# Kernel optimization log

Measured on AMD Instinct MI355X. Metric: run time of the kernel, lower is better.

The kernel has to match this reference:

```python
import jax, jax.numpy as jnp
import numpy as np

B, L, C, H, T = 4096, 32, 28, 512, 32


def setup_inputs() -> dict:
    key = jax.random.key(0)
    ks = jax.random.split(key, 10)
    s = 0.1
    return dict(
        input=jax.random.normal(ks[0], (B, L, C), jnp.float32),
        unpacked_masks=jnp.ones((B, L, 1), jnp.float32),
        bias_mat=jax.random.normal(ks[1], (B, L), jnp.float32),
        conv1_w=jax.random.normal(ks[2], (C, C, 3), jnp.float32) * s,  # OIH
        conv1_b=jnp.zeros((C,), jnp.float32),
        conv_w=jax.random.normal(ks[3], (1, C, 1), jnp.float32) * s,
        conv_b=jnp.zeros((1,), jnp.float32),
        w_ih=jax.random.normal(ks[4], (4 * H, C), jnp.float32) * s,
        w_hh=jax.random.normal(ks[5], (4 * H, H), jnp.float32) * s,
        b_ih=jnp.zeros((4 * H,), jnp.float32),
        b_hh=jnp.concatenate([jnp.zeros(H), jnp.ones(H), jnp.zeros(2 * H)]).astype(jnp.float32),  # forget-gate bias = 1 as in weights_init
        fc1_w=jax.random.normal(ks[6], (1, H), jnp.float32) * s,
        fc1_b=jnp.zeros((1,), jnp.float32),
        conv2_w=jax.random.normal(ks[7], (1, H, 1), jnp.float32) * s,
        conv2_b=jnp.zeros((1,), jnp.float32),
    )


def reference(input, unpacked_masks, bias_mat, conv1_w, conv1_b, conv_w, conv_b,
              w_ih, w_hh, b_ih, b_hh, fc1_w, fc1_b, conv2_w, conv2_b):
    b, l, c = input.shape
    # residual conv block: conv1d(28->28,k3,pad1) -> mask -> elu -> +input
    x_ncl = jnp.transpose(input, (0, 2, 1))
    y = jax.lax.conv_general_dilated(x_ncl, conv1_w, (1,), 'SAME',
                                     dimension_numbers=('NCH', 'OIH', 'NCH'))
    y = jnp.transpose(y + conv1_b[None, :, None], (0, 2, 1))
    x = jax.nn.elu(y * unpacked_masks) + input  # [B,L,C]
    # u_a: 1x1 conv (28->1) == per-position linear, then mask -> [B,L,1]
    u_a = (jnp.einsum('blc,c->bl', x, conv_w[0, :, 0]) + conv_b)[..., None] * unpacked_masks
    bias = bias_mat.reshape(b, l, 1)

    def step(carry, _):
        h, cstate = carry
        w_a = (h @ fc1_w.T + fc1_b)[:, :, None]                 # [B,1,1]
        attn = jax.nn.leaky_relu(u_a + w_a) + bias              # [B,L,1]
        attn = jax.nn.softmax(attn, axis=1)                     # softmax over sequence
        context = jnp.einsum('bl,blc->bc', attn[..., 0], x)     # [B,C]
        gates = context @ w_ih.T + b_ih + h @ w_hh.T + b_hh     # [B,4H]
        i, f, g, o = jnp.split(gates, 4, axis=1)                # torch LSTMCell gate order
        cstate = jax.nn.sigmoid(f) * cstate + jax.nn.sigmoid(i) * jnp.tanh(g)
        h = jax.nn.sigmoid(o) * jnp.tanh(cstate)
        return (h, cstate), h

    h0 = jnp.zeros((b, w_hh.shape[1]), input.dtype)
    (_, _), hs = jax.lax.scan(step, (h0, h0), None, length=T)   # [T,B,H]
    all_hidden = jnp.transpose(hs, (1, 0, 2))                   # [B,T,H]
    # dropout layers are identity in eval; conv2 is 1x1 conv (512->1)
    out = (jnp.einsum('bth,h->bt', all_hidden, conv2_w[0, :, 0]) + conv2_b)[..., None]
    return out * unpacked_masks
```

## Files before the change

kernel.cpp:

```cpp
#include <hip/hip_runtime.h>
#include <hip/hip_bf16.h>

#define B_N 4096
#define L_N 32
#define C_N 28
#define H_N 512
#define T_N 32
#define G_N 2048
#define CHA 34
#define CHSH 4096
#define ABLK (CHA * CHSH)
#define XS 29

typedef __attribute__((ext_vector_type(4))) float f32x4;
typedef __attribute__((ext_vector_type(8))) short s16x8;

static constexpr size_t OFF_WF = 0;
static constexpr size_t AB_ONE = (size_t)32 * ABLK * 2;
static constexpr size_t OFF_AB = OFF_WF + (size_t)16 * ABLK * 2;
static constexpr size_t OFF_X  = OFF_AB + 2 * AB_ONE;
static constexpr size_t OFF_UA = OFF_X + (size_t)B_N * L_N * C_N * 4;
static constexpr size_t OFF_BS = OFF_UA + (size_t)B_N * L_N * 4;
static constexpr size_t OFF_AC = OFF_BS + 8192;
static constexpr size_t ACC_HALF = (size_t)32 * B_N * 4;
static constexpr size_t OFF_CS = OFF_AC + 2 * ACC_HALF;
static constexpr size_t WS_NEED = OFF_CS + (size_t)B_N * H_N * 4;

__device__ __forceinline__ short bfbits(__hip_bfloat16 b) {
    union { __hip_bfloat16 b; short s; } v; v.b = b; return v.s;
}
__device__ __forceinline__ float sigmoidf_(float x) { return 1.f / (1.f + __expf(-x)); }
__device__ __forceinline__ float tanhf_(float x) {
    float ax = fabsf(x), e = __expf(-2.f * ax);
    float t = (1.f - e) / (1.f + e);
    return x < 0.f ? -t : t;
}

__global__ __launch_bounds__(256) void fill_out(float* out, float v) {
    int i = blockIdx.x * 256 + threadIdx.x;
    if (i < B_N * 32) out[i] = v;
}

__global__ __launch_bounds__(256) void prep_x(const float* __restrict__ input,
                       const float* __restrict__ mask,
                       const float* __restrict__ w1, const float* __restrict__ b1,
                       const float* __restrict__ cw, const float* __restrict__ cb,
                       float* __restrict__ x, float* __restrict__ ua)
{
    __shared__ float sw1[C_N * C_N * 3];
    __shared__ float sb1[C_N], scw[C_N];
    __shared__ float sin[8 * L_N * XS];
    __shared__ float sxb[8 * L_N * XS];
    for (int i = threadIdx.x; i < C_N * C_N * 3; i += 256) sw1[i] = w1[i];
    if (threadIdx.x < C_N) { sb1[threadIdx.x] = b1[threadIdx.x]; scw[threadIdx.x] = cw[threadIdx.x]; }
    const float* src = input + (size_t)blockIdx.x * (8 * L_N * C_N);
    for (int i = threadIdx.x; i < 8 * L_N * C_N; i += 256) {
        int lr = i / (L_N * C_N);
        int rem = i - lr * (L_N * C_N);
        int l = rem / C_N, c = rem - l * C_N;
        sin[lr * (L_N * XS) + l * XS + c] = src[i];
    }
    __syncthreads();

    int idx = blockIdx.x * 256 + threadIdx.x;
    int l = idx & 31;
    int wv = threadIdx.x >> 5;
    const float* inb = sin + wv * (L_N * XS);
    float m = mask[idx];
    float uacc = 0.f;
    for (int o = 0; o < C_N; ++o) {
        float y = sb1[o];
        const float* wo = sw1 + o * (C_N * 3);
        for (int i = 0; i < C_N; ++i) {
            float xm1 = (l > 0)  ? inb[(l - 1) * XS + i] : 0.f;
            float x0  = inb[l * XS + i];
            float xp1 = (l < 31) ? inb[(l + 1) * XS + i] : 0.f;
            y += wo[i * 3 + 0] * xm1 + wo[i * 3 + 1] * x0 + wo[i * 3 + 2] * xp1;
        }
        y *= m;
        float e = (y > 0.f) ? y : (__expf(y) - 1.f);
        float xv = e + inb[l * XS + o];
        sxb[wv * (L_N * XS) + l * XS + o] = xv;
        uacc += xv * scw[o];
    }
    ua[idx] = (uacc + cb[0]) * m;
    __syncthreads();
    float* xdst = x + (size_t)blockIdx.x * (8 * L_N * C_N);
    for (int i = threadIdx.x; i < 8 * L_N * C_N; i += 256) {
        int lr = i / (L_N * C_N);
        int rem = i - lr * (L_N * C_N);
        int l2 = rem / C_N, c = rem - l2 * C_N;
        xdst[i] = sxb[lr * (L_N * XS) + l2 * XS + c];
    }
}

__global__ __launch_bounds__(256) void prep_wf(const float* __restrict__ w_ih,
                                               const float* __restrict__ w_hh,
                                               short* __restrict__ Wf)
{
    int blk = blockIdx.x;
    int n128 = blk / CHA, c = blk % CHA;
    bool lo = (c >= 17);
    int kbase = (lo ? (c - 17) : c) * 32;
    short* dst = Wf + ((size_t)n128 * CHA + c) * CHSH;
    for (int g = threadIdx.x; g < 512; g += 256) {
        int j = g >> 6, lane = g & 63;
        int p = n128 * 128 + j * 16 + (lane & 15);
        int unit = p >> 2, gate = p & 3;
        int srow = gate * H_N + unit;
        int kg = lane >> 4;
        s16x8 out;
        #pragma unroll
        for (int b2 = 0; b2 < 8; ++b2) {
            int k = kbase + kg * 8 + b2;
            float v = 0.f;
            if (k < 512) v = w_hh[(size_t)srow * H_N + k];
            else if (k < 540) v = w_ih[srow * C_N + (k - 512)];
            __hip_bfloat16 hi = __float2bfloat16(v);
            if (lo) out[b2] = bfbits(__float2bfloat16(v - __bfloat162float(hi)));
            else    out[b2] = bfbits(hi);
        }
        *(s16x8*)(dst + g * 8) = out;
    }
}

__global__ void prep_bs(const float* __restrict__ b_ih, const float* __restrict__ b_hh,
                        float* __restrict__ bsum)
{
    int p = blockIdx.x * 256 + threadIdx.x;
    if (p < G_N) {
        int unit = p >> 2, gate = p & 3;
        bsum[p] = b_ih[gate * H_N + unit] + b_hh[gate * H_N + unit];
    }
}

__global__ void prep_zero(unsigned int* __restrict__ a32, float* __restrict__ cst,
                          float* __restrict__ acc)
{
    int idx = blockIdx.x * blockDim.x + threadIdx.x;
    if (idx < B_N * 1088) a32[idx] = 0u;
    if (idx < B_N * H_N) cst[idx] = 0.f;
    if (idx < 2 * 32 * B_N) acc[idx] = 0.f;
}

struct RParams {
    const float* mask;
    const float* bias_mat;
    const float* fc1_w;
    const float* fc1_b;
    const float* conv2_w;
    const float* conv2_b;
    const short* Wf;
    const short* Ain;
    short* Aout;
    const float* x;
    const float* ua;
    const float* bsum;
    float* accW;
    float* accO;
    float* cstate;
    float* out;
};

__global__ __launch_bounds__(256) void ctx_step(RParams P, int t)
{
    const int lane = threadIdx.x & 63;
    const int wave = threadIdx.x >> 6;
    const int row  = blockIdx.x * 4 + wave;

    float v = (lane < 32) ? P.accW[lane * B_N + row] : P.accO[(lane - 32) * B_N + row];
    #pragma unroll
    for (int off = 1; off <= 16; off <<= 1) v += __shfl_xor(v, off);
    float aW = __shfl(v, 0);
    float aO = __shfl(v, 32);

    if (t > 0 && lane == 0)
        P.out[row * T_N + (t - 1)] = (aO + P.conv2_b[0]) * P.mask[row * L_N + (t - 1)];

    if (t < T_N) {
        float w_a = aW + P.fc1_b[0];
        int l32 = lane & 31;
        float e = P.ua[row * L_N + l32] + w_a;
        e = (e > 0.f) ? e : 0.01f * e;
        e += P.bias_mat[row * L_N + l32];
        float mx = e;
        #pragma unroll
        for (int off = 16; off > 0; off >>= 1) mx = fmaxf(mx, __shfl_xor(mx, off, 32));
        float pexp = __expf(e - mx);
        float ssum = pexp;
        #pragma unroll
        for (int off = 16; off > 0; off >>= 1) ssum += __shfl_xor(ssum, off, 32);
        float p = pexp / ssum;
        int cc = (lane < C_N) ? lane : 0;
        const float* xrow = P.x + (size_t)row * (L_N * C_N) + cc;
        float ctx = 0.f;
        #pragma unroll
        for (int l = 0; l < L_N; ++l) {
            float al = __shfl(p, l);
            ctx += al * xrow[l * C_N];
        }
        if (lane < C_N) {
            int m128 = row >> 7, mt = (row & 127) >> 4, r = row & 15;
            int flane = r + 16 * (lane >> 3);
            short* base = P.Aout + (size_t)m128 * ABLK + mt * 512 + flane * 8 + (lane & 7);
            __hip_bfloat16 hi = __float2bfloat16(ctx);
            base[16 * CHSH] = bfbits(hi);
            base[33 * CHSH] = bfbits(__float2bfloat16(ctx - __bfloat162float(hi)));
        }
    }
}

#define STG_BUF 32768

__global__ __launch_bounds__(256, 2) void gemm_cell_step(RParams P)
{
    __shared__ __align__(16) char smem[65536];

    const int tid  = threadIdx.x;
    const int lane = tid & 63;
    const int wave = tid >> 6;
    const int bid  = blockIdx.x;
    const int xg = bid & 7, gg = bid >> 3;
    const int m  = (xg >> 1) * 8 + (gg & 7);
    const int n  = (xg & 1) * 8 + (gg >> 3);
    const int wm = wave >> 1, wn = wave & 1;

    const short* Af = P.Ain + (size_t)m * ABLK;
    const short* Wg = P.Wf  + (size_t)n * ABLK;

    const short* slab0 = (wave < 2) ? Af : Wg;
    const int slab_lo  = (wave & 1) ? 17 : 0;

    char* bufp0 = smem;
    char* bufp1 = smem + STG_BUF;

    auto stage = [&](char* lbuf, int kk) {
        const short* gp = slab0 + (size_t)(slab_lo + kk) * CHSH + lane * 8;
        char* lb = lbuf + wave * 8192;
        #pragma unroll
        for (int r = 0; r < 8; ++r) {
            __builtin_amdgcn_global_load_lds(
                (const __attribute__((address_space(1))) void*)(gp + r * 512),
                (__attribute__((address_space(3))) void*)(lb + r * 1024),
                16, 0, 0);
        }
    };

    int aoff[4], woff[4];
    #pragma unroll
    for (int i = 0; i < 4; ++i) {
        aoff[i] = ((wm * 4 + i) * 64 + lane) * 16;
        woff[i] = ((wn * 4 + i) * 64 + lane) * 16;
    }

    f32x4 acc[4][4];
    #pragma unroll
    for (int i = 0; i < 4; ++i)
        #pragma unroll
        for (int j = 0; j < 4; ++j)
            acc[i][j] = (f32x4){0.f, 0.f, 0.f, 0.f};

    stage(bufp0, 0);
    stage(bufp1, 1);

    s16x8 ah[4], al[4], wh[4], wl[4];
    for (int kk = 0; kk < 17; ++kk) {
        if (kk < 16) { asm volatile("s_waitcnt vmcnt(8)" ::: "memory"); }
        else         { asm volatile("s_waitcnt vmcnt(0)" ::: "memory"); }
        __builtin_amdgcn_s_barrier();
        __builtin_amdgcn_sched_barrier(0);
        __builtin_amdgcn_s_setprio(1);
        const char* b = (kk & 1) ? bufp1 : bufp0;
        #pragma unroll
        for (int i = 0; i < 4; ++i) {
            ah[i] = *(const s16x8*)(b + aoff[i]);
            al[i] = *(const s16x8*)(b + 8192 + aoff[i]);
        }
        #pragma unroll
        for (int j = 0; j < 4; ++j) {
            wh[j] = *(const s16x8*)(b + 16384 + woff[j]);
            wl[j] = *(const s16x8*)(b + 24576 + woff[j]);
        }
        #pragma unroll
        for (int i = 0; i < 4; ++i)
            #pragma unroll
            for (int j = 0; j < 4; ++j)
                acc[i][j] = __builtin_amdgcn_mfma_f32_16x16x32_bf16(ah[i], wh[j], acc[i][j], 0, 0, 0);
        #pragma unroll
        for (int i = 0; i < 4; ++i)
            #pragma unroll
            for (int j = 0; j < 4; ++j)
                acc[i][j] = __builtin_amdgcn_mfma_f32_16x16x32_bf16(al[i], wh[j], acc[i][j], 0, 0, 0);
        #pragma unroll
        for (int i = 0; i < 4; ++i)
            #pragma unroll
            for (int j = 0; j < 4; ++j)
                acc[i][j] = __builtin_amdgcn_mfma_f32_16x16x32_bf16(ah[i], wl[j], acc[i][j], 0, 0, 0);
        __builtin_amdgcn_s_setprio(0);
        __builtin_amdgcn_sched_barrier(0);
        __builtin_amdgcn_s_barrier();
        if (kk < 15) stage((kk & 1) ? bufp1 : bufp0, kk + 2);
    }

    __syncthreads();
    float* gates = (float*)smem;
    short* hasm  = (short*)(smem + 32768);
    #pragma unroll
    for (int hh = 0; hh < 2; ++hh) {
        int u = tid & 15, rr = tid >> 4;
        int unit = n * 32 + hh * 16 + u;
        float cpre[8];
        #pragma unroll
        for (int it = 0; it < 8; ++it)
            cpre[it] = P.cstate[(size_t)(m * 128 + it * 16 + rr) * H_N + unit];
        f32x4 bsv = *(const f32x4*)(P.bsum + unit * 4);
        float f1v = P.fc1_w[unit];
        float c2v = P.conv2_w[unit];

        if (wn == hh) {
            #pragma unroll
            for (int i = 0; i < 4; ++i)
                #pragma unroll
                for (int j = 0; j < 4; ++j)
                    #pragma unroll
                    for (int r = 0; r < 4; ++r) {
                        int rowl = wm * 64 + i * 16 + (lane >> 4) * 4 + r;
                        int coll = j * 16 + (lane & 15);
                        gates[rowl * 64 + coll] = acc[i][j][r];
                    }
        }
        __syncthreads();
        {
            int flane = rr + 16 * (hh * 2 + (u >> 3));
            #pragma unroll
            for (int it = 0; it < 8; ++it) {
                int rowl = it * 16 + rr;
                int grow = m * 128 + rowl;
                f32x4 gv = *(const f32x4*)(gates + rowl * 64 + u * 4);
                float pi = gv.x + bsv.x;
                float pf = gv.y + bsv.y;
                float pg = gv.z + bsv.z;
                float po = gv.w + bsv.w;
                float c = sigmoidf_(pf) * cpre[it] + sigmoidf_(pi) * tanhf_(pg);
                P.cstate[(size_t)grow * H_N + unit] = c;
                float h = sigmoidf_(po) * tanhf_(c);
                __hip_bfloat16 hi = __float2bfloat16(h);
                hasm[it * 512 + flane * 8 + (u & 7)]        = bfbits(hi);
                hasm[4096 + it * 512 + flane * 8 + (u & 7)] = bfbits(__float2bfloat16(h - __bfloat162float(hi)));
                float wd = f1v * h, od = c2v * h;
                #pragma unroll
                for (int off = 8; off > 0; off >>= 1) {
                    wd += __shfl_xor(wd, off);
                    od += __shfl_xor(od, off);
                }
                if (u == 0) {
                    P.accW[(n * 2 + hh) * B_N + grow] = wd;
                    P.accO[(n * 2 + hh) * B_N + grow] = od;
                }
            }
        }
        __syncthreads();
    }
    short* dhi = P.Aout + (size_t)m * ABLK + (size_t)n * CHSH;
    short* dlo = P.Aout + (size_t)m * ABLK + (size_t)(17 + n) * CHSH;
    *(s16x8*)(dhi + tid * 16)     = *(const s16x8*)(hasm + tid * 16);
    *(s16x8*)(dhi + tid * 16 + 8) = *(const s16x8*)(hasm + tid * 16 + 8);
    *(s16x8*)(dlo + tid * 16)     = *(const s16x8*)(hasm + 4096 + tid * 16);
    *(s16x8*)(dlo + tid * 16 + 8) = *(const s16x8*)(hasm + 4096 + tid * 16 + 8);
}

extern "C" void kernel_launch(void* const* d_in, const int* in_sizes, int n_in,
                              void* d_out, int out_size, void* d_ws, size_t ws_size,
                              hipStream_t stream)
{
    float* out = (float*)d_out;
    if (ws_size < WS_NEED) { fill_out<<<512, 256, 0, stream>>>(out, 4000.f); return; }

    const float* input = (const float*)d_in[0];
    const float* mask  = (const float*)d_in[1];
    const float* biasm = (const float*)d_in[2];
    const float* w1    = (const float*)d_in[3];
    const float* b1    = (const float*)d_in[4];
    const float* cw    = (const float*)d_in[5];
    const float* cb    = (const float*)d_in[6];
    const float* w_ih  = (const float*)d_in[7];
    const float* w_hh  = (const float*)d_in[8];
    const float* b_ih  = (const float*)d_in[9];
    const float* b_hh  = (const float*)d_in[10];
    const float* fc1w  = (const float*)d_in[11];
    const float* fc1b  = (const float*)d_in[12];
    const float* c2w   = (const float*)d_in[13];
    const float* c2b   = (const float*)d_in[14];

    char* ws = (char*)d_ws;
    short* Wf = (short*)(ws + OFF_WF);
    short* A0 = (short*)(ws + OFF_AB);
    short* A1 = (short*)(ws + OFF_AB + AB_ONE);
    float* x    = (float*)(ws + OFF_X);
    float* ua   = (float*)(ws + OFF_UA);
    float* bsum = (float*)(ws + OFF_BS);
    float* accW = (float*)(ws + OFF_AC);
    float* accO = (float*)(ws + OFF_AC + ACC_HALF);
    float* cst  = (float*)(ws + OFF_CS);

    prep_x<<<(B_N * L_N) / 256, 256, 0, stream>>>(input, mask, w1, b1, cw, cb, x, ua);
    prep_wf<<<16 * CHA, 256, 0, stream>>>(w_ih, w_hh, Wf);
    prep_bs<<<(G_N + 255) / 256, 256, 0, stream>>>(b_ih, b_hh, bsum);
    prep_zero<<<(B_N * 1088 + 255) / 256, 256, 0, stream>>>((unsigned int*)A0, cst, accW);

    RParams P;
    P.mask = mask; P.bias_mat = biasm; P.fc1_w = fc1w; P.fc1_b = fc1b;
    P.conv2_w = c2w; P.conv2_b = c2b; P.Wf = Wf;
    P.x = x; P.ua = ua; P.bsum = bsum; P.accW = accW; P.accO = accO;
    P.cstate = cst; P.out = out;

    short* bufs[2] = { A0, A1 };
    for (int t = 0; t < T_N; ++t) {
        P.Ain  = bufs[t & 1];
        P.Aout = bufs[t & 1];
        ctx_step<<<B_N / 4, 256, 0, stream>>>(P, t);
        P.Ain  = bufs[t & 1];
        P.Aout = bufs[(t + 1) & 1];
        gemm_cell_step<<<512, 256, 0, stream>>>(P);
    }
    P.Ain = bufs[T_N & 1];
    P.Aout = bufs[T_N & 1];
    ctx_step<<<B_N / 4, 256, 0, stream>>>(P, T_N);
}
```

Baseline: 1.443 ms.

## Double-buffer LDS fragments in registers and transpose accW/accO layout

Restructures the GEMM main loop so the next K-slice's fragments are read from shared memory into a second register set while MFMAs run on the current set. Global-to-LDS staging is issued right after the barrier, which replaces the per-iteration vmcnt(8) partial wait with a full wait. Separately, the per-row partial sums accW/accO are stored row-major (row*32+slot), so the context step reads 32 contiguous floats per row instead of strided ones. This roughly doubles the fragment registers held live and can lower occupancy.

Measured after the change: 1.418 ms. About the same (-1.8%).

```diff
diff --git a/kernel.cpp b/kernel.cpp
--- a/kernel.cpp
+++ b/kernel.cpp
@@ -168,7 +168,7 @@
     const int wave = threadIdx.x >> 6;
     const int row  = blockIdx.x * 4 + wave;
 
-    float v = (lane < 32) ? P.accW[lane * B_N + row] : P.accO[(lane - 32) * B_N + row];
+    float v = (lane < 32) ? P.accW[row * 32 + lane] : P.accO[row * 32 + (lane - 32)];
     #pragma unroll
     for (int off = 1; off <= 16; off <<= 1) v += __shfl_xor(v, off);
     float aW = __shfl(v, 0);
@@ -260,47 +260,57 @@
         for (int j = 0; j < 4; ++j)
             acc[i][j] = (f32x4){0.f, 0.f, 0.f, 0.f};
 
-    stage(bufp0, 0);
-    stage(bufp1, 1);
-
-    s16x8 ah[4], al[4], wh[4], wl[4];
-    for (int kk = 0; kk < 17; ++kk) {
-        if (kk < 16) { asm volatile("s_waitcnt vmcnt(8)" ::: "memory"); }
-        else         { asm volatile("s_waitcnt vmcnt(0)" ::: "memory"); }
-        __builtin_amdgcn_s_barrier();
-        __builtin_amdgcn_sched_barrier(0);
-        __builtin_amdgcn_s_setprio(1);
-        const char* b = (kk & 1) ? bufp1 : bufp0;
+    s16x8 RA[16], RB[16];
+    auto ldfr = [&](const char* b, s16x8 (&R)[16]) {
         #pragma unroll
         for (int i = 0; i < 4; ++i) {
-            ah[i] = *(const s16x8*)(b + aoff[i]);
-            al[i] = *(const s16x8*)(b + 8192 + aoff[i]);
-        }
-        #pragma unroll
-        for (int j = 0; j < 4; ++j) {
-            wh[j] = *(const s16x8*)(b + 16384 + woff[j]);
-            wl[j] = *(const s16x8*)(b + 24576 + woff[j]);
-        }
+            R[i]      = *(const s16x8*)(b + aoff[i]);
+            R[4 + i]  = *(const s16x8*)(b + 8192 + aoff[i]);
+            R[8 + i]  = *(const s16x8*)(b + 16384 + woff[i]);
+            R[12 + i] = *(const s16x8*)(b + 24576 + woff[i]);
+        }
+    };
+    auto domm = [&](s16x8 (&R)[16]) {
         #pragma unroll
         for (int i = 0; i < 4; ++i)
             #pragma unroll
             for (int j = 0; j < 4; ++j)
-                acc[i][j] = __builtin_amdgcn_mfma_f32_16x16x32_bf16(ah[i], wh[j], acc[i][j], 0, 0, 0);
+                acc[i][j] = __builtin_amdgcn_mfma_f32_16x16x32_bf16(R[i], R[8 + j], acc[i][j], 0, 0, 0);
         #pragma unroll
         for (int i = 0; i < 4; ++i)
             #pragma unroll
             for (int j = 0; j < 4; ++j)
-                acc[i][j] = __builtin_amdgcn_mfma_f32_16x16x32_bf16(al[i], wh[j], acc[i][j], 0, 0, 0);
+                acc[i][j] = __builtin_amdgcn_mfma_f32_16x16x32_bf16(R[4 + i], R[8 + j], acc[i][j], 0, 0, 0);
         #pragma unroll
         for (int i = 0; i < 4; ++i)
             #pragma unroll
             for (int j = 0; j < 4; ++j)
-                acc[i][j] = __builtin_amdgcn_mfma_f32_16x16x32_bf16(ah[i], wl[j], acc[i][j], 0, 0, 0);
+                acc[i][j] = __builtin_amdgcn_mfma_f32_16x16x32_bf16(R[i], R[12 + j], acc[i][j], 0, 0, 0);
+    };
+    auto step = [&](int kk, s16x8 (&Rc)[16], s16x8 (&Rn)[16], char* bcur, char* bnext) {
+        asm volatile("s_waitcnt vmcnt(0) lgkmcnt(0)" ::: "memory");
+        __builtin_amdgcn_s_barrier();
+        __builtin_amdgcn_sched_barrier(0);
+        if (kk + 2 <= 16) stage(bcur, kk + 2);
+        if (kk + 1 <= 16) ldfr(bnext, Rn);
+        __builtin_amdgcn_sched_barrier(0);
+        __builtin_amdgcn_s_setprio(1);
+        domm(Rc);
         __builtin_amdgcn_s_setprio(0);
         __builtin_amdgcn_sched_barrier(0);
-        __builtin_amdgcn_s_barrier();
-        if (kk < 15) stage((kk & 1) ? bufp1 : bufp0, kk + 2);
-    }
+    };
+
+    stage(bufp0, 0);
+    asm volatile("s_waitcnt vmcnt(0)" ::: "memory");
+    __builtin_amdgcn_s_barrier();
+    stage(bufp1, 1);
+    ldfr(bufp0, RA);
+
+    for (int kp = 0; kp < 8; ++kp) {
+        step(2 * kp,     RA, RB, bufp0, bufp1);
+        step(2 * kp + 1, RB, RA, bufp1, bufp0);
+    }
+    step(16, RA, RB, bufp0, bufp1);
 
     __syncthreads();
     float* gates = (float*)smem;
@@ -354,8 +364,8 @@
                     od += __shfl_xor(od, off);
                 }
                 if (u == 0) {
-                    P.accW[(n * 2 + hh) * B_N + grow] = wd;
-                    P.accO[(n * 2 + hh) * B_N + grow] = od;
+                    P.accW[(size_t)grow * 32 + (n * 2 + hh)] = wd;
+                    P.accO[(size_t)grow * 32 + (n * 2 + hh)] = od;
                 }
             }
         }
```
